# Optimization experiments

Measured on AMD Instinct MI355X. Metric: run time of the kernel, lower is better.

## Reference

```python
import jax, jax.numpy as jnp
import numpy as np

N_NODES = 50000
N_EDGES = 600000
D = 128
BN_EPS = 1e-5


def _linear_init(key, fan_in, fan_out):
    # torch nn.Linear default: U(-1/sqrt(fan_in), 1/sqrt(fan_in)) for W and b
    kw, kb = jax.random.split(key)
    bound = 1.0 / np.sqrt(fan_in)
    W = jax.random.uniform(kw, (fan_in, fan_out), minval=-bound, maxval=bound, dtype=jnp.float32)
    b = jax.random.uniform(kb, (fan_out,), minval=-bound, maxval=bound, dtype=jnp.float32)
    return W, b


def setup_inputs() -> dict:
    key = jax.random.key(0)
    ks = jax.random.split(key, 8)
    x = jax.random.normal(ks[0], (N_NODES, D), dtype=jnp.float32)
    edge_index = jax.random.randint(ks[1], (2, N_EDGES), 0, N_NODES, dtype=jnp.int32)
    edge_attr = jax.random.normal(ks[2], (N_EDGES, D), dtype=jnp.float32)
    # MLP: [2D, D, D, D] -> Linear(2D,D)+SiLU+BN, Linear(D,D)+SiLU+BN, Linear(D,D)
    W1, b1 = _linear_init(ks[3], 2 * D, D)
    W2, b2 = _linear_init(ks[4], D, D)
    W3, b3 = _linear_init(ks[5], D, D)
    g1 = jnp.ones((D,), jnp.float32); be1 = jnp.zeros((D,), jnp.float32)
    g2 = jnp.ones((D,), jnp.float32); be2 = jnp.zeros((D,), jnp.float32)
    return {"x": x, "edge_index": edge_index, "edge_attr": edge_attr,
            "W1": W1, "b1": b1, "g1": g1, "be1": be1,
            "W2": W2, "b2": b2, "g2": g2, "be2": be2,
            "W3": W3, "b3": b3}


def _bn(h, gamma, beta):
    # BatchNorm1d in training mode: normalize with batch statistics (biased var)
    mean = jnp.mean(h, axis=0)
    var = jnp.var(h, axis=0)
    return (h - mean) * jax.lax.rsqrt(var + BN_EPS) * gamma + beta


def reference(x, edge_index, edge_attr, W1, b1, g1, be1, W2, b2, g2, be2, W3, b3):
    src = edge_index[0]
    # scatter_add over edges indexed by source node -> [N_NODES, D]
    agg = jax.ops.segment_sum(edge_attr, src, num_segments=x.shape[0])
    h = jnp.concatenate([x, agg], axis=1)  # [N, 2D]
    h = _bn(jax.nn.silu(h @ W1 + b1), g1, be1)
    h = _bn(jax.nn.silu(h @ W2 + b2), g2, be2)
    return h @ W3 + b3
```

## Files before the change

### kernel.cpp

```cpp
#include <hip/hip_runtime.h>
#include <hip/hip_bf16.h>

#define D 128

typedef __attribute__((ext_vector_type(8))) short bfrag;
typedef __attribute__((ext_vector_type(4))) float facc;
typedef __attribute__((ext_vector_type(4))) unsigned int u32x4;
typedef __attribute__((ext_vector_type(2))) unsigned int u32x2;
typedef __attribute__((ext_vector_type(4))) float f32x4;

__device__ __forceinline__ facc mfma16(bfrag a, bfrag b, facc c) {
    return __builtin_amdgcn_mfma_f32_16x16x32_bf16(a, b, c, 0, 0, 0);
}
__device__ __forceinline__ unsigned int bf16_rn(float f) {
    unsigned int u = __float_as_uint(f);
    u += 0x7FFF + ((u >> 16) & 1);
    return u >> 16;
}
__device__ __forceinline__ float bf16_f(unsigned int h) {
    return __uint_as_float(h << 16);
}
__device__ __forceinline__ unsigned int packf(float v) {
    unsigned int hi = bf16_rn(v);
    unsigned int lo = bf16_rn(v - bf16_f(hi));
    return (hi << 16) | lo;
}
__device__ __forceinline__ float bf16lo(unsigned int u) {
    return __uint_as_float(u << 16);
}
__device__ __forceinline__ float bf16hi(unsigned int u) {
    return __uint_as_float(u & 0xFFFF0000u);
}

__global__ __launch_bounds__(256) void prep_kernel(
    const int* __restrict__ src, int* __restrict__ counts, int nedges,
    const float* __restrict__ x, unsigned int* __restrict__ xp, int n4,
    const float* __restrict__ W1, unsigned short* __restrict__ Wh,
    unsigned short* __restrict__ Wl, int eblk, int sblk) {
    int b = blockIdx.x;
    if (b < eblk) {
        int e = b * 256 + threadIdx.x;
        if (e < nedges) atomicAdd(&counts[src[e]], 1);
    } else if (b < eblk + sblk) {
        int i = (b - eblk) * 256 + threadIdx.x;
        if (i < n4) {
            float4 v = ((const float4*)x)[i];
            uint4 p;
            p.x = packf(v.x);
            p.y = packf(v.y);
            p.z = packf(v.z);
            p.w = packf(v.w);
            ((uint4*)xp)[i] = p;
        }
    } else {
        int j = b - eblk - sblk;
        int k = threadIdx.x;
        float w = W1[(size_t)k * D + j];
        unsigned int hi = bf16_rn(w);
        size_t o = (size_t)((k >> 3) * 128 + j) * 8 + (k & 7);
        Wh[o] = (unsigned short)hi;
        Wl[o] = (unsigned short)bf16_rn(w - bf16_f(hi));
    }
}

#define SCHUNK 2048
__global__ __launch_bounds__(256) void scan1_kernel(
    const int* __restrict__ counts, int* __restrict__ bsum, int n) {
    __shared__ int sd[256];
    const int tid = threadIdx.x;
    const int base = blockIdx.x * SCHUNK + tid * 8;
    int s = 0;
#pragma unroll
    for (int j = 0; j < 8; ++j) {
        int idx = base + j;
        if (idx < n) s += counts[idx];
    }
    sd[tid] = s;
    __syncthreads();
    for (int d2 = 128; d2; d2 >>= 1) {
        if (tid < d2) sd[tid] += sd[tid + d2];
        __syncthreads();
    }
    if (tid == 0) bsum[blockIdx.x] = sd[0];
}
__global__ void scan2_kernel(int* __restrict__ bsum, int nb) {
    int tid = threadIdx.x;
    int v = (tid < nb) ? bsum[tid] : 0;
#pragma unroll
    for (int d2 = 1; d2 < 64; d2 <<= 1) {
        int t = __shfl_up(v, d2);
        if (tid >= d2) v += t;
    }
    if (tid < nb) bsum[tid] = v;
}
__global__ __launch_bounds__(256) void scan3_kernel(
    const int* __restrict__ counts, const int* __restrict__ bsum,
    int* __restrict__ off, int* __restrict__ cur, int n) {
    __shared__ int sd[256];
    const int tid = threadIdx.x;
    const int base = blockIdx.x * SCHUNK + tid * 8;
    int loc[8];
    int s = 0;
#pragma unroll
    for (int j = 0; j < 8; ++j) {
        int idx = base + j;
        int c = (idx < n) ? counts[idx] : 0;
        loc[j] = c;
        s += c;
    }
    sd[tid] = s;
    __syncthreads();
#pragma unroll
    for (int d2 = 1; d2 < 256; d2 <<= 1) {
        int t = (tid >= d2) ? sd[tid - d2] : 0;
        __syncthreads();
        sd[tid] += t;
        __syncthreads();
    }
    int boff = (blockIdx.x == 0) ? 0 : bsum[blockIdx.x - 1];
    int pre = boff + sd[tid] - s;
#pragma unroll
    for (int j = 0; j < 8; ++j) {
        int idx = base + j;
        if (idx < n) {
            off[idx] = pre;
            cur[idx] = pre;
            pre += loc[j];
        }
    }
    if (tid == 255 && base + 8 >= n && n <= blockIdx.x * SCHUNK + SCHUNK)
        off[n] = boff + sd[255];
}

__global__ __launch_bounds__(256) void fillp_kernel(
    const float* __restrict__ edge_attr, const int* __restrict__ src,
    int* __restrict__ cur, unsigned int* __restrict__ ebS, int nedges) {
    const int l = threadIdx.x & 63;
    const int h = l >> 5;
    const int c = l & 31;
    const int e0 = blockIdx.x * 16 + (threadIdx.x >> 6) * 2 + h;
#pragma unroll
    for (int rep = 0; rep < 2; ++rep) {
        int e = e0 + rep * 8;
        if (e >= nedges) continue;
        f32x4 v = __builtin_nontemporal_load(
            (const f32x4*)(edge_attr + (size_t)e * D) + c);
        int slot = 0;
        if (c == 0) slot = atomicAdd(&cur[src[e]], 1);
        slot = __shfl(slot, l & 32);
        u32x2 p;
        p.x = bf16_rn(v[0]) | (bf16_rn(v[1]) << 16);
        p.y = bf16_rn(v[2]) | (bf16_rn(v[3]) << 16);
        *((u32x2*)(ebS + (size_t)slot * 64) + c) = p;
    }
}

__global__ __launch_bounds__(256) void gatherS_kernel(
    const unsigned int* __restrict__ ebS, const int* __restrict__ off,
    unsigned int* __restrict__ aggp, int nnodes) {
    int node = blockIdx.x * 4 + (threadIdx.x >> 6);
    int lane = threadIdx.x & 63;
    if (node >= nnodes) return;
    const int h = lane >> 5;
    const int c = lane & 31;
    int i = off[node];
    const int e = off[node + 1];
    f32x4 acc = {0.f, 0.f, 0.f, 0.f};
    for (; i + 8 <= e; i += 8) {
        u32x2 q[4];
#pragma unroll
        for (int u = 0; u < 4; ++u)
            q[u] = __builtin_nontemporal_load(
                (const u32x2*)(ebS + (size_t)(i + 2 * u + h) * 64) + c);
#pragma unroll
        for (int u = 0; u < 4; ++u) {
            acc[0] += bf16lo(q[u].x);
            acc[1] += bf16hi(q[u].x);
            acc[2] += bf16lo(q[u].y);
            acc[3] += bf16hi(q[u].y);
        }
    }
    for (; i + 2 <= e; i += 2) {
        u32x2 q = __builtin_nontemporal_load(
            (const u32x2*)(ebS + (size_t)(i + h) * 64) + c);
        acc[0] += bf16lo(q.x);
        acc[1] += bf16hi(q.x);
        acc[2] += bf16lo(q.y);
        acc[3] += bf16hi(q.y);
    }
    if (i < e && h == 0) {
        u32x2 q = __builtin_nontemporal_load(
            (const u32x2*)(ebS + (size_t)i * 64) + c);
        acc[0] += bf16lo(q.x);
        acc[1] += bf16hi(q.x);
        acc[2] += bf16lo(q.y);
        acc[3] += bf16hi(q.y);
    }
#pragma unroll
    for (int r = 0; r < 4; ++r) acc[r] += __shfl_xor(acc[r], 32);
    if (h == 0) {
        u32x4 p;
#pragma unroll
        for (int r = 0; r < 4; ++r) p[r] = packf(acc[r]);
        *((u32x4*)(aggp + (size_t)node * D) + c) = p;
    }
}

__global__ void fold_kernel(const float* __restrict__ sum,
                            const float* __restrict__ sq,
                            const float* __restrict__ gamma,
                            const float* __restrict__ beta,
                            const float* __restrict__ W,
                            const float* __restrict__ b,
                            unsigned short* __restrict__ Wh,
                            unsigned short* __restrict__ Wl,
                            float* __restrict__ bf, float invM) {
    int j = blockIdx.x;
    int k = threadIdx.x;
    float mean = sum[k] * invM;
    float var = sq[k] * invM - mean * mean;
    float scale = gamma[k] * rsqrtf(var + 1e-5f);
    float shift = beta[k] - mean * scale;
    float w = W[k * D + j];
    float wf = scale * w;
    unsigned int hi = bf16_rn(wf);
    size_t o = (size_t)((k >> 3) * 128 + j) * 8 + (k & 7);
    Wh[o] = (unsigned short)hi;
    Wl[o] = (unsigned short)bf16_rn(wf - bf16_f(hi));
    float v = shift * w;
#pragma unroll
    for (int of = 32; of; of >>= 1) v += __shfl_down(v, of);
    __shared__ float ws2[2];
    if ((k & 63) == 0) ws2[k >> 6] = v;
    __syncthreads();
    if (k == 0) bf[j] = b[j] + ws2[0] + ws2[1];
}

template <int K, bool SILU, bool STATS, bool PACKOUT>
__global__ __launch_bounds__(256, 2) void gemm_mfma(
    const unsigned int* __restrict__ A0, const unsigned int* __restrict__ A1,
    const unsigned short* __restrict__ Wh,
    const unsigned short* __restrict__ Wl,
    const float* __restrict__ bias, unsigned int* __restrict__ Cp,
    float* __restrict__ Cf, float* __restrict__ gsum,
    float* __restrict__ gsq, int M) {
    constexpr int NS = K / 32;
    const int tid = threadIdx.x;
    const int w = tid >> 6;
    const int l = tid & 63;
    const int lr = l & 15;
    const int lk = l >> 4;
    const int row0 = blockIdx.x * 128 + w * 32;

    facc acc[2][8];
#pragma unroll
    for (int rt = 0; rt < 2; ++rt)
#pragma unroll
        for (int ct = 0; ct < 8; ++ct)
#pragma unroll
            for (int r = 0; r < 4; ++r) acc[rt][ct][r] = 0.f;

    for (int s = 0; s < NS; ++s) {
        const int kb = s * 32 + lk * 8;
        bfrag ah[2], al[2];
#pragma unroll
        for (int rt = 0; rt < 2; ++rt) {
            const int arow = row0 + rt * 16 + lr;
            const unsigned int* As = A0;
            int kk = kb;
            if (K == 256 && s >= 4) { As = A1; kk = kb - 128; }
            u32x4 q0 = {0u, 0u, 0u, 0u}, q1 = {0u, 0u, 0u, 0u};
            if (arow < M) {
                const u32x4* p = (const u32x4*)(As + (size_t)arow * D + kk);
                q0 = p[0];
                q1 = p[1];
            }
            unsigned int ua[8] = {q0.x, q0.y, q0.z, q0.w,
                                  q1.x, q1.y, q1.z, q1.w};
            u32x4 uh, ul;
#pragma unroll
            for (int r = 0; r < 4; ++r) {
                uh[r] = __builtin_amdgcn_perm(ua[2 * r + 1], ua[2 * r],
                                              0x07060302u);
                ul[r] = __builtin_amdgcn_perm(ua[2 * r + 1], ua[2 * r],
                                              0x05040100u);
            }
            ah[rt] = __builtin_bit_cast(bfrag, uh);
            al[rt] = __builtin_bit_cast(bfrag, ul);
        }
        bfrag bh[8], bl[8];
        const int fb = (s * 4 + lk) * 128;
#pragma unroll
        for (int ct = 0; ct < 8; ++ct) {
            size_t o = (size_t)(fb + ct * 16 + lr) * 8;
            bh[ct] = *(const bfrag*)(Wh + o);
            bl[ct] = *(const bfrag*)(Wl + o);
        }
#pragma unroll
        for (int rt = 0; rt < 2; ++rt)
#pragma unroll
            for (int ct = 0; ct < 8; ++ct)
                acc[rt][ct] = mfma16(ah[rt], bh[ct], acc[rt][ct]);
#pragma unroll
        for (int rt = 0; rt < 2; ++rt)
#pragma unroll
            for (int ct = 0; ct < 8; ++ct)
                acc[rt][ct] = mfma16(ah[rt], bl[ct], acc[rt][ct]);
#pragma unroll
        for (int rt = 0; rt < 2; ++rt)
#pragma unroll
            for (int ct = 0; ct < 8; ++ct)
                acc[rt][ct] = mfma16(al[rt], bh[ct], acc[rt][ct]);
    }

    __shared__ float sred[2][4][128];
#pragma unroll
    for (int ct = 0; ct < 8; ++ct) {
        const int col = ct * 16 + lr;
        const float bj = bias[col];
        float s = 0.f, q = 0.f;
#pragma unroll
        for (int rt = 0; rt < 2; ++rt) {
            const int base = row0 + rt * 16 + lk * 4;
#pragma unroll
            for (int r = 0; r < 4; ++r) {
                int crow = base + r;
                if (crow < M) {
                    float v = acc[rt][ct][r] + bj;
                    if (SILU) v = v / (1.0f + __expf(-v));
                    if (PACKOUT) Cp[(size_t)crow * D + col] = packf(v);
                    else         Cf[(size_t)crow * D + col] = v;
                    if (STATS) { s += v; q += v * v; }
                }
            }
        }
        if (STATS) {
            s += __shfl_xor(s, 16);
            s += __shfl_xor(s, 32);
            q += __shfl_xor(q, 16);
            q += __shfl_xor(q, 32);
            if (lk == 0) {
                sred[0][w][col] = s;
                sred[1][w][col] = q;
            }
        }
    }
    if (STATS) {
        __syncthreads();
        if (tid < 128) {
            float v = sred[0][0][tid] + sred[0][1][tid] + sred[0][2][tid] +
                      sred[0][3][tid];
            unsafeAtomicAdd(&gsum[tid], v);
        } else {
            int c = tid - 128;
            float v = sred[1][0][c] + sred[1][1][c] + sred[1][2][c] +
                      sred[1][3][c];
            unsafeAtomicAdd(&gsq[c], v);
        }
    }
}

extern "C" void kernel_launch(void* const* d_in, const int* in_sizes, int n_in,
                              void* d_out, int out_size, void* d_ws,
                              size_t ws_size, hipStream_t stream) {
    const float* x     = (const float*)d_in[0];
    const int*   eidx  = (const int*)d_in[1];
    const float* eattr = (const float*)d_in[2];
    const float* W1  = (const float*)d_in[3];
    const float* b1  = (const float*)d_in[4];
    const float* g1  = (const float*)d_in[5];
    const float* be1 = (const float*)d_in[6];
    const float* W2  = (const float*)d_in[7];
    const float* b2  = (const float*)d_in[8];
    const float* g2  = (const float*)d_in[9];
    const float* be2 = (const float*)d_in[10];
    const float* W3  = (const float*)d_in[11];
    const float* b3  = (const float*)d_in[12];

    const int M = in_sizes[0] / D;
    const int E = in_sizes[1] / 2;
    const int* srcIdx = eidx;

    unsigned int* wsu = (unsigned int*)d_ws;
    unsigned int* ebS = wsu;
    unsigned int* xp  = ebS + (size_t)E * 64;
    unsigned int* h1p = xp + (size_t)M * D;
    unsigned int* h2p = h1p + (size_t)M * D;
    float* sum1 = (float*)(h2p + (size_t)M * D);
    float* sq1  = sum1 + D;
    float* sum2 = sq1 + D;
    float* sq2  = sum2 + D;
    float* b2f  = sq2 + D;
    float* b3f  = b2f + D;
    int* counts = (int*)(b3f + D);
    int* off    = counts + M;
    int* cur    = off + M + 4;
    int* bsum   = cur + M;
    unsigned short* W1h = (unsigned short*)(bsum + 64);
    unsigned short* W1l = W1h + 256 * D;
    unsigned short* W2h = W1l + 256 * D;
    unsigned short* W2l = W2h + D * D;
    unsigned short* W3h = W2l + D * D;
    unsigned short* W3l = W3h + D * D;

    unsigned int* aggp = h2p;

    float* out = (float*)d_out;

    (void)hipMemsetAsync(counts, 0, (size_t)M * sizeof(int), stream);
    (void)hipMemsetAsync(sum1, 0, 4 * D * sizeof(float), stream);

    const int eblk = (E + 255) / 256;
    const int sblk = (M * 32 + 255) / 256;
    prep_kernel<<<eblk + sblk + 128, 256, 0, stream>>>(
        srcIdx, counts, E, x, xp, M * 32, W1, W1h, W1l, eblk, sblk);

    const int nb = (M + SCHUNK - 1) / SCHUNK;
    scan1_kernel<<<nb, 256, 0, stream>>>(counts, bsum, M);
    scan2_kernel<<<1, 64, 0, stream>>>(bsum, nb);
    scan3_kernel<<<nb, 256, 0, stream>>>(counts, bsum, off, cur, M);

    fillp_kernel<<<(E + 15) / 16, 256, 0, stream>>>(eattr, srcIdx, cur, ebS, E);

    gatherS_kernel<<<(M + 3) / 4, 256, 0, stream>>>(ebS, off, aggp, M);

    int nblk = (M + 127) / 128;
    gemm_mfma<256, true, true, true><<<nblk, 256, 0, stream>>>(
        xp, aggp, W1h, W1l, b1, h1p, nullptr, sum1, sq1, M);
    fold_kernel<<<D, D, 0, stream>>>(sum1, sq1, g1, be1, W2, b2, W2h, W2l,
                                     b2f, 1.0f / (float)M);
    gemm_mfma<128, true, true, true><<<nblk, 256, 0, stream>>>(
        h1p, nullptr, W2h, W2l, b2f, h2p, nullptr, sum2, sq2, M);
    fold_kernel<<<D, D, 0, stream>>>(sum2, sq2, g2, be2, W3, b3, W3h, W3l,
                                     b3f, 1.0f / (float)M);
    gemm_mfma<128, false, false, false><<<nblk, 256, 0, stream>>>(
        h2p, nullptr, W3h, W3l, b3f, nullptr, out, nullptr, nullptr, M);
}
```

Baseline: 258.2 us.

## Bucket edges by node block and aggregate in shared memory with LDS atomics

Replaces the per-node counting sort (per-node histogram, three-kernel scan, per-node fill and segment gather) with a coarse bucketing by blocks of 64 nodes. A shared-memory histogram cuts global atomics, a single-block scan replaces the three scan kernels, and each bucket's edges are summed into a 64x128 fp32 LDS tile with shared atomics before being written out. This removes two kernel launches and much of the global atomic traffic, but adds a 16-bit local id per edge and replaces register accumulation with contended LDS float atomics. Summation order also becomes nondeterministic.

```diff
diff --git a/kernel.cpp b/kernel.cpp
--- a/kernel.cpp
+++ b/kernel.cpp
@@ -2,6 +2,8 @@
 #include <hip/hip_bf16.h>
 
 #define D 128
+#define BN 64
+#define MAXNB 1024
 
 typedef __attribute__((ext_vector_type(8))) short bfrag;
 typedef __attribute__((ext_vector_type(4))) float facc;
@@ -33,16 +35,27 @@
 }
 
 __global__ __launch_bounds__(256) void prep_kernel(
-    const int* __restrict__ src, int* __restrict__ counts, int nedges,
-    const float* __restrict__ x, unsigned int* __restrict__ xp, int n4,
-    const float* __restrict__ W1, unsigned short* __restrict__ Wh,
-    unsigned short* __restrict__ Wl, int eblk, int sblk) {
+    const int* __restrict__ src, int* __restrict__ bcounts, int nedges,
+    int nb, const float* __restrict__ x, unsigned int* __restrict__ xp,
+    int n4, const float* __restrict__ W1, unsigned short* __restrict__ Wh,
+    unsigned short* __restrict__ Wl, int hblk, int sblk) {
     int b = blockIdx.x;
-    if (b < eblk) {
-        int e = b * 256 + threadIdx.x;
-        if (e < nedges) atomicAdd(&counts[src[e]], 1);
-    } else if (b < eblk + sblk) {
-        int i = (b - eblk) * 256 + threadIdx.x;
+    int tid = threadIdx.x;
+    if (b < hblk) {
+        __shared__ int hbin[MAXNB];
+        for (int i = tid; i < nb; i += 256) hbin[i] = 0;
+        __syncthreads();
+        int base = b * 2048 + tid * 8;
+#pragma unroll
+        for (int j = 0; j < 8; ++j) {
+            int e = base + j;
+            if (e < nedges) atomicAdd(&hbin[src[e] / BN], 1);
+        }
+        __syncthreads();
+        for (int i = tid; i < nb; i += 256)
+            if (hbin[i]) atomicAdd(&bcounts[i], hbin[i]);
+    } else if (b < hblk + sblk) {
+        int i = (b - hblk) * 256 + tid;
         if (i < n4) {
             float4 v = ((const float4*)x)[i];
             uint4 p;
@@ -53,8 +66,8 @@
             ((uint4*)xp)[i] = p;
         }
     } else {
-        int j = b - eblk - sblk;
-        int k = threadIdx.x;
+        int j = b - hblk - sblk;
+        int k = tid;
         float w = W1[(size_t)k * D + j];
         unsigned int hi = bf16_rn(w);
         size_t o = (size_t)((k >> 3) * 128 + j) * 8 + (k & 7);
@@ -63,51 +76,16 @@
     }
 }
 
-#define SCHUNK 2048
-__global__ __launch_bounds__(256) void scan1_kernel(
-    const int* __restrict__ counts, int* __restrict__ bsum, int n) {
+__global__ __launch_bounds__(256) void scanB_kernel(
+    const int* __restrict__ bcounts, int* __restrict__ boff,
+    int* __restrict__ bcur, int nb, int nedges) {
     __shared__ int sd[256];
     const int tid = threadIdx.x;
-    const int base = blockIdx.x * SCHUNK + tid * 8;
+    const int per = (nb + 255) / 256;
+    const int lo = min(tid * per, nb);
+    const int hi = min(lo + per, nb);
     int s = 0;
-#pragma unroll
-    for (int j = 0; j < 8; ++j) {
-        int idx = base + j;
-        if (idx < n) s += counts[idx];
-    }
-    sd[tid] = s;
-    __syncthreads();
-    for (int d2 = 128; d2; d2 >>= 1) {
-        if (tid < d2) sd[tid] += sd[tid + d2];
-        __syncthreads();
-    }
-    if (tid == 0) bsum[blockIdx.x] = sd[0];
-}
-__global__ void scan2_kernel(int* __restrict__ bsum, int nb) {
-    int tid = threadIdx.x;
-    int v = (tid < nb) ? bsum[tid] : 0;
-#pragma unroll
-    for (int d2 = 1; d2 < 64; d2 <<= 1) {
-        int t = __shfl_up(v, d2);
-        if (tid >= d2) v += t;
-    }
-    if (tid < nb) bsum[tid] = v;
-}
-__global__ __launch_bounds__(256) void scan3_kernel(
-    const int* __restrict__ counts, const int* __restrict__ bsum,
-    int* __restrict__ off, int* __restrict__ cur, int n) {
-    __shared__ int sd[256];
-    const int tid = threadIdx.x;
-    const int base = blockIdx.x * SCHUNK + tid * 8;
-    int loc[8];
-    int s = 0;
-#pragma unroll
-    for (int j = 0; j < 8; ++j) {
-        int idx = base + j;
-        int c = (idx < n) ? counts[idx] : 0;
-        loc[j] = c;
-        s += c;
-    }
+    for (int i = lo; i < hi; ++i) s += bcounts[i];
     sd[tid] = s;
     __syncthreads();
 #pragma unroll
@@ -117,24 +95,19 @@
         sd[tid] += t;
         __syncthreads();
     }
-    int boff = (blockIdx.x == 0) ? 0 : bsum[blockIdx.x - 1];
-    int pre = boff + sd[tid] - s;
-#pragma unroll
-    for (int j = 0; j < 8; ++j) {
-        int idx = base + j;
-        if (idx < n) {
-            off[idx] = pre;
-            cur[idx] = pre;
-            pre += loc[j];
-        }
-    }
-    if (tid == 255 && base + 8 >= n && n <= blockIdx.x * SCHUNK + SCHUNK)
-        off[n] = boff + sd[255];
-}
-
-__global__ __launch_bounds__(256) void fillp_kernel(
+    int pre = (tid == 0) ? 0 : sd[tid - 1];
+    for (int i = lo; i < hi; ++i) {
+        boff[i] = pre;
+        bcur[i] = pre;
+        pre += bcounts[i];
+    }
+    if (tid == 255) boff[nb] = nedges;
+}
+
+__global__ __launch_bounds__(256) void passA_kernel(
     const float* __restrict__ edge_attr, const int* __restrict__ src,
-    int* __restrict__ cur, unsigned int* __restrict__ ebS, int nedges) {
+    int* __restrict__ bcur, unsigned int* __restrict__ ebB,
+    unsigned short* __restrict__ lid16, int nedges) {
     const int l = threadIdx.x & 63;
     const int h = l >> 5;
     const int c = l & 31;
@@ -146,63 +119,81 @@
         f32x4 v = __builtin_nontemporal_load(
             (const f32x4*)(edge_attr + (size_t)e * D) + c);
         int slot = 0;
-        if (c == 0) slot = atomicAdd(&cur[src[e]], 1);
+        if (c == 0) {
+            int s = src[e];
+            int b = s / BN;
+            slot = atomicAdd(&bcur[b], 1);
+            lid16[slot] = (unsigned short)(s - b * BN);
+        }
         slot = __shfl(slot, l & 32);
         u32x2 p;
         p.x = bf16_rn(v[0]) | (bf16_rn(v[1]) << 16);
         p.y = bf16_rn(v[2]) | (bf16_rn(v[3]) << 16);
-        *((u32x2*)(ebS + (size_t)slot * 64) + c) = p;
-    }
-}
-
-__global__ __launch_bounds__(256) void gatherS_kernel(
-    const unsigned int* __restrict__ ebS, const int* __restrict__ off,
-    unsigned int* __restrict__ aggp, int nnodes) {
-    int node = blockIdx.x * 4 + (threadIdx.x >> 6);
-    int lane = threadIdx.x & 63;
-    if (node >= nnodes) return;
-    const int h = lane >> 5;
-    const int c = lane & 31;
-    int i = off[node];
-    const int e = off[node + 1];
-    f32x4 acc = {0.f, 0.f, 0.f, 0.f};
-    for (; i + 8 <= e; i += 8) {
+        *((u32x2*)(ebB + (size_t)slot * 64) + c) = p;
+    }
+}
+
+__global__ __launch_bounds__(256) void passB_kernel(
+    const unsigned int* __restrict__ ebB,
+    const unsigned short* __restrict__ lid16, const int* __restrict__ boff,
+    unsigned int* __restrict__ aggp, int M) {
+    __shared__ float sagg[BN * D];
+    const int tid = threadIdx.x;
+    const int b = blockIdx.x;
+    {
+        float4* z = (float4*)sagg;
+        for (int i = tid; i < BN * D / 4; i += 256)
+            z[i] = make_float4(0.f, 0.f, 0.f, 0.f);
+    }
+    __syncthreads();
+
+    const int base = boff[b];
+    const int end = boff[b + 1];
+    const int hw = ((tid >> 6) << 1) | ((tid & 63) >> 5);
+    const int c = tid & 31;
+
+    int r = base + hw;
+    for (; r + 24 < end; r += 32) {
         u32x2 q[4];
-#pragma unroll
-        for (int u = 0; u < 4; ++u)
+        int lv[4];
+#pragma unroll
+        for (int u = 0; u < 4; ++u) {
+            int rr = r + u * 8;
             q[u] = __builtin_nontemporal_load(
-                (const u32x2*)(ebS + (size_t)(i + 2 * u + h) * 64) + c);
+                (const u32x2*)(ebB + (size_t)rr * 64) + c);
+            lv[u] = lid16[rr];
+        }
 #pragma unroll
         for (int u = 0; u < 4; ++u) {
-            acc[0] += bf16lo(q[u].x);
-            acc[1] += bf16hi(q[u].x);
-            acc[2] += bf16lo(q[u].y);
-            acc[3] += bf16hi(q[u].y);
-        }
-    }
-    for (; i + 2 <= e; i += 2) {
+            float* sg = &sagg[lv[u] * D + 4 * c];
+            atomicAdd(sg + 0, bf16lo(q[u].x));
+            atomicAdd(sg + 1, bf16hi(q[u].x));
+            atomicAdd(sg + 2, bf16lo(q[u].y));
+            atomicAdd(sg + 3, bf16hi(q[u].y));
+        }
+    }
+    for (; r < end; r += 8) {
         u32x2 q = __builtin_nontemporal_load(
-            (const u32x2*)(ebS + (size_t)(i + h) * 64) + c);
-        acc[0] += bf16lo(q.x);
-        acc[1] += bf16hi(q.x);
-        acc[2] += bf16lo(q.y);
-        acc[3] += bf16hi(q.y);
-    }
-    if (i < e && h == 0) {
-        u32x2 q = __builtin_nontemporal_load(
-            (const u32x2*)(ebS + (size_t)i * 64) + c);
-        acc[0] += bf16lo(q.x);
-        acc[1] += bf16hi(q.x);
-        acc[2] += bf16lo(q.y);
-        acc[3] += bf16hi(q.y);
-    }
-#pragma unroll
-    for (int r = 0; r < 4; ++r) acc[r] += __shfl_xor(acc[r], 32);
-    if (h == 0) {
-        u32x4 p;
-#pragma unroll
-        for (int r = 0; r < 4; ++r) p[r] = packf(acc[r]);
-        *((u32x4*)(aggp + (size_t)node * D) + c) = p;
+            (const u32x2*)(ebB + (size_t)r * 64) + c);
+        float* sg = &sagg[lid16[r] * D + 4 * c];
+        atomicAdd(sg + 0, bf16lo(q.x));
+        atomicAdd(sg + 1, bf16hi(q.x));
+        atomicAdd(sg + 2, bf16lo(q.y));
+        atomicAdd(sg + 3, bf16hi(q.y));
+    }
+    __syncthreads();
+
+    for (int idx = tid; idx < BN * 32; idx += 256) {
+        int nl = idx >> 5;
+        int cc = idx & 31;
+        int g = b * BN + nl;
+        if (g < M) {
+            u32x4 p;
+#pragma unroll
+            for (int u = 0; u < 4; ++u)
+                p[u] = packf(sagg[nl * D + cc * 4 + u]);
+            *((u32x4*)(aggp + (size_t)g * D) + cc) = p;
+        }
     }
 }
 
@@ -380,10 +371,11 @@
     const int M = in_sizes[0] / D;
     const int E = in_sizes[1] / 2;
     const int* srcIdx = eidx;
+    const int nb = (M + BN - 1) / BN;
 
     unsigned int* wsu = (unsigned int*)d_ws;
-    unsigned int* ebS = wsu;
-    unsigned int* xp  = ebS + (size_t)E * 64;
+    unsigned int* ebB = wsu;
+    unsigned int* xp  = ebB + (size_t)E * 64;
     unsigned int* h1p = xp + (size_t)M * D;
     unsigned int* h2p = h1p + (size_t)M * D;
     float* sum1 = (float*)(h2p + (size_t)M * D);
@@ -392,37 +384,34 @@
     float* sq2  = sum2 + D;
     float* b2f  = sq2 + D;
     float* b3f  = b2f + D;
-    int* counts = (int*)(b3f + D);
-    int* off    = counts + M;
-    int* cur    = off + M + 4;
-    int* bsum   = cur + M;
-    unsigned short* W1h = (unsigned short*)(bsum + 64);
+    int* bcounts = (int*)(b3f + D);
+    int* boff    = bcounts + nb;
+    int* bcur    = boff + nb + 4;
+    unsigned short* W1h = (unsigned short*)(bcur + nb);
     unsigned short* W1l = W1h + 256 * D;
     unsigned short* W2h = W1l + 256 * D;
     unsigned short* W2l = W2h + D * D;
     unsigned short* W3h = W2l + D * D;
     unsigned short* W3l = W3h + D * D;
+    unsigned short* lid16 = W3l + D * D;
 
     unsigned int* aggp = h2p;
 
     float* out = (float*)d_out;
 
-    (void)hipMemsetAsync(counts, 0, (size_t)M * sizeof(int), stream);
+    (void)hipMemsetAsync(bcounts, 0, (size_t)nb * sizeof(int), stream);
     (void)hipMemsetAsync(sum1, 0, 4 * D * sizeof(float), stream);
 
-    const int eblk = (E + 255) / 256;
+    const int hblk = (E + 2047) / 2048;
     const int sblk = (M * 32 + 255) / 256;
-    prep_kernel<<<eblk + sblk + 128, 256, 0, stream>>>(
-        srcIdx, counts, E, x, xp, M * 32, W1, W1h, W1l, eblk, sblk);
-
-    const int nb = (M + SCHUNK - 1) / SCHUNK;
-    scan1_kernel<<<nb, 256, 0, stream>>>(counts, bsum, M);
-    scan2_kernel<<<1, 64, 0, stream>>>(bsum, nb);
-    scan3_kernel<<<nb, 256, 0, stream>>>(counts, bsum, off, cur, M);
-
-    fillp_kernel<<<(E + 15) / 16, 256, 0, stream>>>(eattr, srcIdx, cur, ebS, E);
-
-    gatherS_kernel<<<(M + 3) / 4, 256, 0, stream>>>(ebS, off, aggp, M);
+    prep_kernel<<<hblk + sblk + 128, 256, 0, stream>>>(
+        srcIdx, bcounts, E, nb, x, xp, M * 32, W1, W1h, W1l, hblk, sblk);
+
+    scanB_kernel<<<1, 256, 0, stream>>>(bcounts, boff, bcur, nb, E);
+
+    passA_kernel<<<(E + 15) / 16, 256, 0, stream>>>(eattr, srcIdx, bcur, ebB,
+                                                    lid16, E);
+    passB_kernel<<<nb, 256, 0, stream>>>(ebB, lid16, boff, aggp, M);
 
     int nblk = (M + 127) / 128;
     gemm_mfma<256, true, true, true><<<nblk, 256, 0, stream>>>(
```

Result: slower. 875.8 us (+239.2%).
